# Kernel tuning notes

Hardware: AMD Instinct MI355X
Metric: run time of the kernel (lower is better)

## Reference

```python
import jax, jax.numpy as jnp
import numpy as np

B, S, H, E, K, NH = 2, 2048, 1024, 8, 2, 8
HD = H // NH          # head dim = 128
HQ = H // 4           # seasonal encoder width = 256
CAP = int(B * S * 1.5 * K / E)  # expert capacity = 1536


def setup_inputs() -> dict:
    key = jax.random.key(0)
    ks = iter(jax.random.split(key, 32))

    def lin(shape):
        fan_in = shape[0]
        return jax.random.normal(next(ks), shape, jnp.float32) / np.sqrt(fan_in)

    inp = {
        "hidden_states": jax.random.normal(next(ks), (B, S, H), jnp.float32),
        # position embedding table [sequence_length, H]
        "pos_emb": jax.random.normal(next(ks), (S, H), jnp.float32) * 0.02,
        # temporal_encoder: Linear(H+2,H) -> ReLU -> Linear(H,H)
        "We1": lin((H + 2, H)), "be1": jnp.zeros((H,), jnp.float32),
        "We2": lin((H, H)),     "be2": jnp.zeros((H,), jnp.float32),
        # seasonal_encoder: Linear(1,H//4) -> ReLU -> Linear(H//4,H//4)
        "Ws1": lin((1, HQ)),   "bs1": jnp.zeros((HQ,), jnp.float32),
        "Ws2": lin((HQ, HQ)),  "bs2": jnp.zeros((HQ,), jnp.float32),
        # temporal_attention (MultiheadAttention, 8 heads)
        "Wq": lin((H, H)), "bq": jnp.zeros((H,), jnp.float32),
        "Wk": lin((H, H)), "bk": jnp.zeros((H,), jnp.float32),
        "Wv": lin((H, H)), "bv": jnp.zeros((H,), jnp.float32),
        "Wo": lin((H, H)), "bo": jnp.zeros((H,), jnp.float32),
        # temporal_router: Linear(H,H) -> ReLU -> Linear(H,E)
        "Wr1": lin((H, H)), "br1": jnp.zeros((H,), jnp.float32),
        "Wr2": lin((H, E)), "br2": jnp.zeros((E,), jnp.float32),
    }
    return inp


def _forward(hidden_states, pos_emb, We1, be1, We2, be2, Ws1, bs1, Ws2, bs2,
             Wq, bq, Wk, bk, Wv, bv, Wo, bo, Wr1, br1, Wr2, br2):
    b, s, h = hidden_states.shape
    # time features (time_info is None -> defaults)
    t = jnp.arange(s, dtype=jnp.float32)                   # [S]
    season = jnp.sin(t * 2.0 * jnp.pi / 24.0)              # [S]
    time_feat = jnp.broadcast_to(jnp.stack([t, season], -1), (b, s, 2))

    combined = jnp.concatenate([hidden_states, time_feat], axis=-1)  # [B,S,H+2]
    enc = jax.nn.relu(combined @ We1 + be1) @ We2 + be2              # [B,S,H]

    pos = pos_emb[:s]                                                # [S,H]
    seas = jax.nn.relu(season[:, None] @ Ws1 + bs1) @ Ws2 + bs2      # [S,H//4]
    seas_full = jnp.tile(seas, (1, h // seas.shape[-1]))             # [S,H] (expand to H)

    x = enc + pos[None] + seas_full[None]                            # [B,S,H]

    # self-attention (eval mode, no dropout)
    def heads(y):
        return y.reshape(b, s, NH, HD)
    q = heads(x @ Wq + bq)
    k = heads(x @ Wk + bk)
    v = heads(x @ Wv + bv)
    scores = jnp.einsum('bqhd,bkhd->bhqk', q, k) / np.sqrt(HD)
    attn = jax.nn.softmax(scores, axis=-1)
    ctx = jnp.einsum('bhqk,bkhd->bqhd', attn, v).reshape(b, s, h)
    x = ctx @ Wo + bo

    logits = jax.nn.relu(x @ Wr1 + br1) @ Wr2 + br2                  # [B,S,E]
    probs = jax.nn.softmax(logits, axis=-1)

    topv, topi = jax.lax.top_k(probs, K)                             # [B,S,K]
    topv = topv / topv.sum(-1, keepdims=True)

    onehot = jax.nn.one_hot(topi, E, dtype=probs.dtype)              # [B,S,K,E]
    disp0 = onehot.sum(-2)                                           # [B,S,E] (0/1)
    comb0 = (topv[..., None] * onehot).sum(-2)                       # [B,S,E]

    # only capacity slot 0 is ever written (per original code)
    dispatch = jnp.zeros((b, s, E, CAP), probs.dtype).at[..., 0].set(disp0)
    combine = jnp.zeros((b, s, E, CAP), probs.dtype).at[..., 0].set(comb0)

    p_mean = probs.mean(axis=(0, 1))                                 # [E]
    aux_loss = jnp.sum(p_mean * jnp.log(p_mean * E + 1e-9))
    return dispatch, combine, probs, aux_loss


def reference(hidden_states, pos_emb, We1, be1, We2, be2, Ws1, bs1, Ws2, bs2,
              Wq, bq, Wk, bk, Wv, bv, Wo, bo, Wr1, br1, Wr2, br2):
    return _forward(hidden_states, pos_emb, We1, be1, We2, be2, Ws1, bs1, Ws2, bs2,
                    Wq, bq, Wk, bk, Wv, bv, Wo, bo, Wr1, br1, Wr2, br2)
```

## Files before the change

### kernel.cpp

```cpp
#include <hip/hip_runtime.h>
#include <hip/hip_fp16.h>
#include <math.h>

#define N_TOK 4096
#define S_LEN 2048
#define H_DIM 1024
#define E_EXP 8
#define CAPV  1536
#define NHEAD 8
#define HDHD  128

#define SCRATCH_F4 2129920u
#define TOTAL_F4   25165824u

typedef __attribute__((ext_vector_type(8))) _Float16 v8h;
typedef __attribute__((ext_vector_type(4))) float v4f;

__device__ __forceinline__ void splitf16(float v, unsigned short& h, unsigned short& l) {
    __half hh = __float2half(v);
    h = __half_as_ushort(hh);
    l = __half_as_ushort(__float2half(v - __half2float(hh)));
}

__device__ __forceinline__ void gld_lds16(const void* g, void* l) {
    __builtin_amdgcn_global_load_lds(
        (const __attribute__((address_space(1))) unsigned int*)g,
        (__attribute__((address_space(3))) unsigned int*)l,
        16, 0, 0);
}

__global__ __launch_bounds__(256) void prep_k(
    const float* __restrict__ hid, unsigned short* __restrict__ hi,
    unsigned short* __restrict__ lo,
    const float* __restrict__ Ws1, const float* __restrict__ bs1,
    const float* __restrict__ Ws2, const float* __restrict__ bs2,
    float* __restrict__ seasons, float* __restrict__ seas24,
    const float* __restrict__ Wr2, float* __restrict__ wr2t) {
    __shared__ float hbuf[256];
    int blk = blockIdx.x;
    int tid = threadIdx.x;
    if (blk < 4096) {
        int i = blk * 256 + tid;
        float4 v = ((const float4*)hid)[i];
        ushort4 h, l;
        splitf16(v.x, h.x, l.x);
        splitf16(v.y, h.y, l.y);
        splitf16(v.z, h.z, l.z);
        splitf16(v.w, h.w, l.w);
        ((ushort4*)hi)[i] = h;
        ((ushort4*)lo)[i] = l;
    } else if (blk < 4104) {
        int s = (blk - 4096) * 256 + tid;
        if (s < S_LEN) {
            double a = (double)s * 2.0 * M_PI / 24.0;
            seasons[s] = (float)sin(a);
        }
    } else if (blk < 4128) {
        int m = blk - 4104;
        double a = (double)m * 2.0 * M_PI / 24.0;
        float sv = (float)sin(a);
        int j = tid;
        hbuf[j] = fmaxf(sv * Ws1[j] + bs1[j], 0.f);
        __syncthreads();
        float acc = bs2[j];
        for (int i = 0; i < 256; ++i) acc = fmaf(hbuf[i], Ws2[i * 256 + j], acc);
        seas24[m * 256 + j] = acc;
    } else {
        int i = (blk - 4128) * 256 + tid;
        int k = i >> 3, e = i & 7;
        wr2t[e * 1024 + k] = Wr2[i];
    }
}

__device__ __forceinline__ void wconv_body(const float* __restrict__ W,
                                           unsigned short* __restrict__ Thi,
                                           unsigned short* __restrict__ Tlo) {
    __shared__ unsigned short Hs[64][65];
    __shared__ unsigned short Ls[64][65];
    int k0 = blockIdx.y * 64, n0 = blockIdx.x * 64;
    int tid = threadIdx.x;
#pragma unroll
    for (int i = 0; i < 4; ++i) {
        int idx = tid + i * 256;
        int kk = idx >> 4, n4 = idx & 15;
        float4 v = *(const float4*)(W + (size_t)(k0 + kk) * 1024 + n0 + n4 * 4);
        unsigned short h, l;
        splitf16(v.x, h, l); Hs[n4 * 4 + 0][kk] = h; Ls[n4 * 4 + 0][kk] = l;
        splitf16(v.y, h, l); Hs[n4 * 4 + 1][kk] = h; Ls[n4 * 4 + 1][kk] = l;
        splitf16(v.z, h, l); Hs[n4 * 4 + 2][kk] = h; Ls[n4 * 4 + 2][kk] = l;
        splitf16(v.w, h, l); Hs[n4 * 4 + 3][kk] = h; Ls[n4 * 4 + 3][kk] = l;
    }
    __syncthreads();
#pragma unroll
    for (int i = 0; i < 4; ++i) {
        int idx = tid + i * 256;
        int n = idx >> 4, k4 = idx & 15;
        ushort4 h = make_ushort4(Hs[n][k4 * 4], Hs[n][k4 * 4 + 1], Hs[n][k4 * 4 + 2], Hs[n][k4 * 4 + 3]);
        ushort4 l = make_ushort4(Ls[n][k4 * 4], Ls[n][k4 * 4 + 1], Ls[n][k4 * 4 + 2], Ls[n][k4 * 4 + 3]);
        *(ushort4*)(Thi + (size_t)(n0 + n) * 1024 + k0 + k4 * 4) = h;
        *(ushort4*)(Tlo + (size_t)(n0 + n) * 1024 + k0 + k4 * 4) = l;
    }
}

struct WBatch {
    const float* src[7];
    unsigned short* dh[7];
    unsigned short* dl[7];
};

__global__ __launch_bounds__(256) void wconv_batch_k(WBatch wb) {
    int i = blockIdx.z;
    wconv_body(wb.src[i], wb.dh[i], wb.dl[i]);
}

__device__ __forceinline__ void fill_body(float* __restrict__ p, size_t f40, size_t f41, int nblk) {
    v4f z = {0.f, 0.f, 0.f, 0.f};
    v4f* o = (v4f*)p;
    size_t n = f41 - f40;
    for (size_t i = (size_t)blockIdx.x * 256 + threadIdx.x; i < n; i += (size_t)nblk * 256)
        __builtin_nontemporal_store(z, o + f40 + i);
}

template <int MODE, int EMITF, int EMITS, int FILLN>
__global__ __launch_bounds__(256, 2) void gemm_split(
    const unsigned short* __restrict__ Ahi, const unsigned short* __restrict__ Alo,
    const unsigned short* __restrict__ WThi, const unsigned short* __restrict__ WTlo,
    const float* __restrict__ bias, float* __restrict__ Cf,
    unsigned short* __restrict__ Chi, unsigned short* __restrict__ Clo,
    const float* __restrict__ rowT, const float* __restrict__ rowS,
    const float* __restrict__ seasons, const float* __restrict__ pos,
    const float* __restrict__ seas24, float escale, float* __restrict__ fillp) {
    if (FILLN > 0) {
        if (blockIdx.x < (unsigned)FILLN) {
            fill_body(fillp, 0, SCRATCH_F4, FILLN);
            return;
        }
    }
    __shared__ unsigned short Ash[2][128 * 32];
    __shared__ unsigned short Asl[2][128 * 32];
    __shared__ unsigned short Bsh[2][128 * 32];
    __shared__ unsigned short Bsl[2][128 * 32];
    int tid = threadIdx.x;
    int lane = tid & 63, w = tid >> 6;
    int l15 = lane & 15, l16 = lane >> 4;
    int wm = (w >> 1) * 64, wn = (w & 1) * 64;

    int bid = blockIdx.x - FILLN;
    int mp = (bid & 7) + ((bid >> 6) << 3);
    int np = (bid >> 3) & 7;
    int m0 = mp * 128, n0 = np * 128;

    int ac0 = tid, ac1 = tid + 256;
    int ar0 = ac0 >> 2, ar1 = ac1 >> 2;
    size_t a_src0 = (size_t)(m0 + ar0) * 1024 + (((ac0 & 3) ^ (ar0 & 3)) * 8);
    size_t a_src1 = (size_t)(m0 + ar1) * 1024 + (((ac1 & 3) ^ (ar1 & 3)) * 8);
    size_t b_src0 = (size_t)(n0 + ar0) * 1024 + (((ac0 & 3) ^ (ar0 & 3)) * 8);
    size_t b_src1 = (size_t)(n0 + ar1) * 1024 + (((ac1 & 3) ^ (ar1 & 3)) * 8);

    int a_off[4], b_off[4];
#pragma unroll
    for (int mi = 0; mi < 4; ++mi) {
        int row = wm + mi * 16 + l15;
        a_off[mi] = row * 32 + ((l16 ^ (row & 3)) * 8);
    }
#pragma unroll
    for (int ni = 0; ni < 4; ++ni) {
        int n = wn + ni * 16 + l15;
        b_off[ni] = n * 32 + ((l16 ^ (n & 3)) * 8);
    }

    auto STAGE = [&](int buf, int k0) {
        gld_lds16(Ahi + a_src0 + k0, &Ash[buf][ac0 * 8]);
        gld_lds16(Ahi + a_src1 + k0, &Ash[buf][ac1 * 8]);
        gld_lds16(Alo + a_src0 + k0, &Asl[buf][ac0 * 8]);
        gld_lds16(Alo + a_src1 + k0, &Asl[buf][ac1 * 8]);
        gld_lds16(WThi + b_src0 + k0, &Bsh[buf][ac0 * 8]);
        gld_lds16(WThi + b_src1 + k0, &Bsh[buf][ac1 * 8]);
        gld_lds16(WTlo + b_src0 + k0, &Bsl[buf][ac0 * 8]);
        gld_lds16(WTlo + b_src1 + k0, &Bsl[buf][ac1 * 8]);
    };

    v4f acc[4][4] = {};
    STAGE(0, 0);
    __syncthreads();

    for (int kk = 0; kk < 32; ++kk) {
        int cur = kk & 1;
        if (kk < 31) STAGE(cur ^ 1, (kk + 1) * 32);
        v8h ah[4], al[4], bh[4], bl[4];
#pragma unroll
        for (int mi = 0; mi < 4; ++mi) {
            ah[mi] = *(const v8h*)&Ash[cur][a_off[mi]];
            al[mi] = *(const v8h*)&Asl[cur][a_off[mi]];
        }
#pragma unroll
        for (int ni = 0; ni < 4; ++ni) {
            bh[ni] = *(const v8h*)&Bsh[cur][b_off[ni]];
            bl[ni] = *(const v8h*)&Bsl[cur][b_off[ni]];
        }
#pragma unroll
        for (int mi = 0; mi < 4; ++mi)
#pragma unroll
            for (int ni = 0; ni < 4; ++ni) {
                acc[mi][ni] = __builtin_amdgcn_mfma_f32_16x16x32_f16(ah[mi], bh[ni], acc[mi][ni], 0, 0, 0);
                acc[mi][ni] = __builtin_amdgcn_mfma_f32_16x16x32_f16(al[mi], bh[ni], acc[mi][ni], 0, 0, 0);
                acc[mi][ni] = __builtin_amdgcn_mfma_f32_16x16x32_f16(ah[mi], bl[ni], acc[mi][ni], 0, 0, 0);
            }
        __syncthreads();
    }

#pragma unroll
    for (int mi = 0; mi < 4; ++mi) {
#pragma unroll
        for (int r = 0; r < 4; ++r) {
            int row = m0 + wm + mi * 16 + l16 * 4 + r;
            int s = row & (S_LEN - 1);
            float tval = 0.f, seval = 0.f;
            if (MODE == 1) { tval = (float)s; seval = seasons[s]; }
#pragma unroll
            for (int ni = 0; ni < 4; ++ni) {
                int col = n0 + wn + ni * 16 + l15;
                float v = acc[mi][ni][r] + bias[col];
                if (MODE == 1) v += tval * rowT[col] + seval * rowS[col];
                if (MODE == 2) v += pos[(size_t)s * 1024 + col] + seas24[(s % 24) * 256 + (col & 255)];
                if (MODE == 1 || MODE == 3) v = fmaxf(v, 0.f);
                size_t o = (size_t)row * 1024 + col;
                if (EMITF) Cf[o] = v;
                if (EMITS) {
                    unsigned short hu, lu;
                    splitf16(v * escale, hu, lu);
                    Chi[o] = hu; Clo[o] = lu;
                }
            }
        }
    }
}

#define NFILLQ 256
__global__ __launch_bounds__(256, 2) void gemm_qkv(
    const unsigned short* __restrict__ Ahi, const unsigned short* __restrict__ Alo,
    const unsigned short* __restrict__ WT3hi, const unsigned short* __restrict__ WT3lo,
    const float* __restrict__ bq, const float* __restrict__ bk,
    const float* __restrict__ bv,
    unsigned short* __restrict__ Qhi, unsigned short* __restrict__ Qlo,
    unsigned short* __restrict__ Khi, unsigned short* __restrict__ Klo,
    unsigned short* __restrict__ VThi, unsigned short* __restrict__ VTlo,
    float qscale, float* __restrict__ fillp) {
    if (blockIdx.x < NFILLQ) {
        fill_body(fillp, SCRATCH_F4, TOTAL_F4, NFILLQ);
        return;
    }
    __shared__ unsigned short Ash[2][128 * 32];
    __shared__ unsigned short Asl[2][128 * 32];
    __shared__ unsigned short Bsh[2][128 * 32];
    __shared__ unsigned short Bsl[2][128 * 32];
    int tid = threadIdx.x;
    int lane = tid & 63, w = tid >> 6;
    int l15 = lane & 15, l16 = lane >> 4;
    int wm = (w >> 1) * 64, wn = (w & 1) * 64;

    int bid = blockIdx.x - NFILLQ;
    int t = bid >> 3;
    int np = t % 24;
    int mp = (bid & 7) + (t / 24) * 8;
    int m0 = mp * 128;
    int wn0 = np * 128;

    int ac0 = tid, ac1 = tid + 256;
    int ar0 = ac0 >> 2, ar1 = ac1 >> 2;
    size_t a_src0 = (size_t)(m0 + ar0) * 1024 + (((ac0 & 3) ^ (ar0 & 3)) * 8);
    size_t a_src1 = (size_t)(m0 + ar1) * 1024 + (((ac1 & 3) ^ (ar1 & 3)) * 8);
    size_t b_src0 = (size_t)(wn0 + ar0) * 1024 + (((ac0 & 3) ^ (ar0 & 3)) * 8);
    size_t b_src1 = (size_t)(wn0 + ar1) * 1024 + (((ac1 & 3) ^ (ar1 & 3)) * 8);

    int a_off[4], b_off[4];
#pragma unroll
    for (int mi = 0; mi < 4; ++mi) {
        int row = wm + mi * 16 + l15;
        a_off[mi] = row * 32 + ((l16 ^ (row & 3)) * 8);
    }
#pragma unroll
    for (int ni = 0; ni < 4; ++ni) {
        int n = wn + ni * 16 + l15;
        b_off[ni] = n * 32 + ((l16 ^ (n & 3)) * 8);
    }

    auto STAGE = [&](int buf, int k0) {
        gld_lds16(Ahi + a_src0 + k0, &Ash[buf][ac0 * 8]);
        gld_lds16(Ahi + a_src1 + k0, &Ash[buf][ac1 * 8]);
        gld_lds16(Alo + a_src0 + k0, &Asl[buf][ac0 * 8]);
        gld_lds16(Alo + a_src1 + k0, &Asl[buf][ac1 * 8]);
        gld_lds16(WT3hi + b_src0 + k0, &Bsh[buf][ac0 * 8]);
        gld_lds16(WT3hi + b_src1 + k0, &Bsh[buf][ac1 * 8]);
        gld_lds16(WT3lo + b_src0 + k0, &Bsl[buf][ac0 * 8]);
        gld_lds16(WT3lo + b_src1 + k0, &Bsl[buf][ac1 * 8]);
    };

    v4f acc[4][4] = {};
    STAGE(0, 0);
    __syncthreads();

    for (int kk = 0; kk < 32; ++kk) {
        int cur = kk & 1;
        if (kk < 31) STAGE(cur ^ 1, (kk + 1) * 32);
        v8h ah[4], al[4], bh[4], bl[4];
#pragma unroll
        for (int mi = 0; mi < 4; ++mi) {
            ah[mi] = *(const v8h*)&Ash[cur][a_off[mi]];
            al[mi] = *(const v8h*)&Asl[cur][a_off[mi]];
        }
#pragma unroll
        for (int ni = 0; ni < 4; ++ni) {
            bh[ni] = *(const v8h*)&Bsh[cur][b_off[ni]];
            bl[ni] = *(const v8h*)&Bsl[cur][b_off[ni]];
        }
#pragma unroll
        for (int mi = 0; mi < 4; ++mi)
#pragma unroll
            for (int ni = 0; ni < 4; ++ni) {
                acc[mi][ni] = __builtin_amdgcn_mfma_f32_16x16x32_f16(ah[mi], bh[ni], acc[mi][ni], 0, 0, 0);
                acc[mi][ni] = __builtin_amdgcn_mfma_f32_16x16x32_f16(al[mi], bh[ni], acc[mi][ni], 0, 0, 0);
                acc[mi][ni] = __builtin_amdgcn_mfma_f32_16x16x32_f16(ah[mi], bl[ni], acc[mi][ni], 0, 0, 0);
            }
        __syncthreads();
    }

    if (np >= 16) {
        int n0 = (np - 16) * 128;
#pragma unroll
        for (int mi = 0; mi < 4; ++mi) {
            int row0 = m0 + wm + mi * 16 + l16 * 4;
            int bb = row0 >> 11, ss = row0 & 2047;
#pragma unroll
            for (int ni = 0; ni < 4; ++ni) {
                int col = n0 + wn + ni * 16 + l15;
                int hh = col >> 7, dd = col & 127;
                size_t base = ((size_t)((bb * 8 + hh) * 128 + dd)) * 2048 + ss;
                ushort4 vh, vl;
                float v0 = acc[mi][ni][0] + bv[col];
                float v1 = acc[mi][ni][1] + bv[col];
                float v2 = acc[mi][ni][2] + bv[col];
                float v3 = acc[mi][ni][3] + bv[col];
                splitf16(v0, vh.x, vl.x);
                splitf16(v1, vh.y, vl.y);
                splitf16(v2, vh.z, vl.z);
                splitf16(v3, vh.w, vl.w);
                *(ushort4*)(VThi + base) = vh;
                *(ushort4*)(VTlo + base) = vl;
            }
        }
    } else {
        const float* bias = np < 8 ? bq : bk;
        unsigned short* Dhi = np < 8 ? Qhi : Khi;
        unsigned short* Dlo = np < 8 ? Qlo : Klo;
        float esc = np < 8 ? qscale : 1.f;
        int n0 = (np & 7) * 128;
#pragma unroll
        for (int mi = 0; mi < 4; ++mi) {
#pragma unroll
            for (int r = 0; r < 4; ++r) {
                int row = m0 + wm + mi * 16 + l16 * 4 + r;
#pragma unroll
                for (int ni = 0; ni < 4; ++ni) {
                    int col = n0 + wn + ni * 16 + l15;
                    float v = (acc[mi][ni][r] + bias[col]) * esc;
                    size_t o = (size_t)row * 1024 + col;
                    unsigned short hu, lu;
                    splitf16(v, hu, lu);
                    Dhi[o] = hu; Dlo[o] = lu;
                }
            }
        }
    }
}

__global__ __launch_bounds__(256, 4) void attn_mfma_k(
    const unsigned short* __restrict__ qhi, const unsigned short* __restrict__ qlo,
    const unsigned short* __restrict__ khi, const unsigned short* __restrict__ klo,
    const unsigned short* __restrict__ vthi, const unsigned short* __restrict__ vtlo,
    float* __restrict__ OP, float* __restrict__ ML) {
    __shared__ unsigned short Ks_hi[32 * 128];
    __shared__ unsigned short Ks_lo[32 * 128];
    __shared__ unsigned short Vs_hi[128 * 32];
    __shared__ unsigned short Vs_lo[128 * 32];
    __shared__ unsigned int   Ps[64 * 32];

    int p = blockIdx.x;
    int x = (p >> 3) & 31;
    int g = (p & 7) + ((p >> 8) << 3);
    int bh = g >> 1, z = g & 1;
    int b = bh >> 3, h = bh & 7;
    int q0 = x * 64;
    int tid = threadIdx.x;
    int lane = tid & 63, w = tid >> 6;
    int l15 = lane & 15, l16 = lane >> 4;
    int wm = w * 16;

    v8h qa_h[4], qa_l[4];
    {
        size_t qrow = (size_t)(b * S_LEN + q0 + wm + l15) * H_DIM + h * HDHD;
#pragma unroll
        for (int ks = 0; ks < 4; ++ks) {
            qa_h[ks] = *(const v8h*)(qhi + qrow + ks * 32 + l16 * 8);
            qa_l[ks] = *(const v8h*)(qlo + qrow + ks * 32 + l16 * 8);
        }
    }

    int ktok1 = tid >> 4, kslot1 = tid & 15;
    int ktok2 = ktok1 + 16;
    size_t ksrc1 = (size_t)(b * S_LEN + ktok1) * H_DIM + h * HDHD + ((kslot1 ^ (ktok1 & 7)) * 8);
    size_t ksrc2 = (size_t)(b * S_LEN + ktok2) * H_DIM + h * HDHD + ((kslot1 ^ (ktok2 & 7)) * 8);
    int vd1 = tid >> 2, vslot1 = tid & 3;
    int vd2 = vd1 + 64;
    size_t vsrc1 = (size_t)(bh * HDHD + vd1) * S_LEN + ((vslot1 ^ ((vd1 >> 1) & 3)) * 8);
    size_t vsrc2 = (size_t)(bh * HDHD + vd2) * S_LEN + ((vslot1 ^ ((vd2 >> 1) & 3)) * 8);

    v4f accO[8] = {};
    float mreg[4] = {-1e30f, -1e30f, -1e30f, -1e30f};
    float lreg[4] = {};

    int kt0 = z * 1024;
    for (int it = 0; it < 32; ++it) {
        int kt = kt0 + it * 32;
        __syncthreads();
        size_t koff = (size_t)kt * H_DIM;
        gld_lds16(khi + ksrc1 + koff, &Ks_hi[tid * 8]);
        gld_lds16(khi + ksrc2 + koff, &Ks_hi[(tid + 256) * 8]);
        gld_lds16(klo + ksrc1 + koff, &Ks_lo[tid * 8]);
        gld_lds16(klo + ksrc2 + koff, &Ks_lo[(tid + 256) * 8]);
        gld_lds16(vthi + vsrc1 + kt, &Vs_hi[tid * 8]);
        gld_lds16(vthi + vsrc2 + kt, &Vs_hi[(tid + 256) * 8]);
        gld_lds16(vtlo + vsrc1 + kt, &Vs_lo[tid * 8]);
        gld_lds16(vtlo + vsrc2 + kt, &Vs_lo[(tid + 256) * 8]);
        __syncthreads();

        v4f s0 = {}, s1 = {};
#pragma unroll
        for (int ks = 0; ks < 4; ++ks) {
#pragma unroll
            for (int nt = 0; nt < 2; ++nt) {
                int tok = nt * 16 + l15;
                int slot = (ks * 4 + l16) ^ (tok & 7);
                v8h bhf = *(const v8h*)&Ks_hi[tok * 128 + slot * 8];
                v8h blf = *(const v8h*)&Ks_lo[tok * 128 + slot * 8];
                v4f& ss = nt ? s1 : s0;
                ss = __builtin_amdgcn_mfma_f32_16x16x32_f16(qa_h[ks], bhf, ss, 0, 0, 0);
                ss = __builtin_amdgcn_mfma_f32_16x16x32_f16(qa_l[ks], bhf, ss, 0, 0, 0);
                ss = __builtin_amdgcn_mfma_f32_16x16x32_f16(qa_h[ks], blf, ss, 0, 0, 0);
            }
        }

        float p0[4], p1[4], alpha[4];
#pragma unroll
        for (int r = 0; r < 4; ++r) {
            float tmax = fmaxf(s0[r], s1[r]);
            tmax = fmaxf(tmax, __shfl_xor(tmax, 1));
            tmax = fmaxf(tmax, __shfl_xor(tmax, 2));
            tmax = fmaxf(tmax, __shfl_xor(tmax, 4));
            tmax = fmaxf(tmax, __shfl_xor(tmax, 8));
            float mnew = fmaxf(mreg[r], tmax);
            alpha[r] = __expf(mreg[r] - mnew);
            p0[r] = __expf(s0[r] - mnew);
            p1[r] = __expf(s1[r] - mnew);
            float lt = p0[r] + p1[r];
            lt += __shfl_xor(lt, 1);
            lt += __shfl_xor(lt, 2);
            lt += __shfl_xor(lt, 4);
            lt += __shfl_xor(lt, 8);
            lreg[r] = lreg[r] * alpha[r] + lt;
            mreg[r] = mnew;
        }
#pragma unroll
        for (int nt = 0; nt < 8; ++nt)
#pragma unroll
            for (int r = 0; r < 4; ++r) accO[nt][r] *= alpha[r];

#pragma unroll
        for (int r = 0; r < 4; ++r) {
            int qq = wm + l16 * 4 + r;
            unsigned short ph, pl;
            splitf16(p0[r], ph, pl);
            int k0i = l15;
            Ps[qq * 32 + ((((k0i >> 2) ^ (qq & 7)) << 2) | (k0i & 3))] =
                (unsigned)ph | ((unsigned)pl << 16);
            splitf16(p1[r], ph, pl);
            int k1i = 16 + l15;
            Ps[qq * 32 + ((((k1i >> 2) ^ (qq & 7)) << 2) | (k1i & 3))] =
                (unsigned)ph | ((unsigned)pl << 16);
        }

        int qq = wm + l15;
        int sA = (l16 * 2) ^ (qq & 7);
        int sB = (l16 * 2 + 1) ^ (qq & 7);
        uint4 ua = *(const uint4*)&Ps[qq * 32 + sA * 4];
        uint4 ub = *(const uint4*)&Ps[qq * 32 + sB * 4];
        uint4 ahw, alw;
        ahw.x = (ua.x & 0xffffu) | (ua.y << 16);
        ahw.y = (ua.z & 0xffffu) | (ua.w << 16);
        ahw.z = (ub.x & 0xffffu) | (ub.y << 16);
        ahw.w = (ub.z & 0xffffu) | (ub.w << 16);
        alw.x = (ua.x >> 16) | (ua.y & 0xffff0000u);
        alw.y = (ua.z >> 16) | (ua.w & 0xffff0000u);
        alw.z = (ub.x >> 16) | (ub.y & 0xffff0000u);
        alw.w = (ub.z >> 16) | (ub.w & 0xffff0000u);
        v8h pA_h = __builtin_bit_cast(v8h, ahw);
        v8h pA_l = __builtin_bit_cast(v8h, alw);
#pragma unroll
        for (int nt = 0; nt < 8; ++nt) {
            int d = nt * 16 + l15;
            int slot = l16 ^ ((d >> 1) & 3);
            v8h vhf = *(const v8h*)&Vs_hi[d * 32 + slot * 8];
            v8h vlf = *(const v8h*)&Vs_lo[d * 32 + slot * 8];
            accO[nt] = __builtin_amdgcn_mfma_f32_16x16x32_f16(pA_h, vhf, accO[nt], 0, 0, 0);
            accO[nt] = __builtin_amdgcn_mfma_f32_16x16x32_f16(pA_l, vhf, accO[nt], 0, 0, 0);
            accO[nt] = __builtin_amdgcn_mfma_f32_16x16x32_f16(pA_h, vlf, accO[nt], 0, 0, 0);
        }
    }

#pragma unroll
    for (int r = 0; r < 4; ++r) {
        if (l15 == 0) {
            int q = q0 + wm + l16 * 4 + r;
            size_t mlo = ((size_t)(z * 16 + bh) * 2048 + q) * 2;
            ML[mlo] = mreg[r];
            ML[mlo + 1] = lreg[r];
        }
    }
#pragma unroll
    for (int nt = 0; nt < 8; ++nt) {
#pragma unroll
        for (int r = 0; r < 4; ++r) {
            int q = q0 + wm + l16 * 4 + r;
            size_t o = ((size_t)(z * 16 + bh) * 2048 + q) * 128 + nt * 16 + l15;
            OP[o] = accO[nt][r];
        }
    }
}

__global__ __launch_bounds__(256) void attn_combine_k(
    const float* __restrict__ OP, const float* __restrict__ ML,
    unsigned short* __restrict__ ctx_hi, unsigned short* __restrict__ ctx_lo) {
    int tid = threadIdx.x;
    int R = blockIdx.x * 16 + (tid >> 4);
    int bh = R >> 11, q = R & 2047;
    int b = bh >> 3, h = bh & 7;
    int d0 = (tid & 15) * 8;
    size_t ml0 = ((size_t)bh * 2048 + q) * 2;
    size_t ml1 = ((size_t)(16 + bh) * 2048 + q) * 2;
    float m0 = ML[ml0], l0 = ML[ml0 + 1];
    float m1 = ML[ml1], l1 = ML[ml1 + 1];
    float m = fmaxf(m0, m1);
    float w0 = __expf(m0 - m), w1 = __expf(m1 - m);
    float inv = 1.f / (w0 * l0 + w1 * l1);
    const float* O0 = OP + ((size_t)bh * 2048 + q) * 128 + d0;
    const float* O1 = OP + ((size_t)(16 + bh) * 2048 + q) * 128 + d0;
    size_t dst = ((size_t)(b * 2048 + q)) * 1024 + h * 128 + d0;
    float4 a0 = *(const float4*)O0;
    float4 a1 = *(const float4*)(O0 + 4);
    float4 c0 = *(const float4*)O1;
    float4 c1 = *(const float4*)(O1 + 4);
    ushort4 h0, h1, lo0, lo1;
    splitf16((w0 * a0.x + w1 * c0.x) * inv, h0.x, lo0.x);
    splitf16((w0 * a0.y + w1 * c0.y) * inv, h0.y, lo0.y);
    splitf16((w0 * a0.z + w1 * c0.z) * inv, h0.z, lo0.z);
    splitf16((w0 * a0.w + w1 * c0.w) * inv, h0.w, lo0.w);
    splitf16((w0 * a1.x + w1 * c1.x) * inv, h1.x, lo1.x);
    splitf16((w0 * a1.y + w1 * c1.y) * inv, h1.y, lo1.y);
    splitf16((w0 * a1.z + w1 * c1.z) * inv, h1.z, lo1.z);
    splitf16((w0 * a1.w + w1 * c1.w) * inv, h1.w, lo1.w);
    *(ushort4*)(ctx_hi + dst) = h0;
    *(ushort4*)(ctx_hi + dst + 4) = h1;
    *(ushort4*)(ctx_lo + dst) = lo0;
    *(ushort4*)(ctx_lo + dst + 4) = lo1;
}

__global__ __launch_bounds__(256) void logits_k(const float* __restrict__ h1,
                                                const float* __restrict__ Wr2T,
                                                const float* __restrict__ br2,
                                                float* __restrict__ logits) {
    __shared__ float part[256];
    int tid = threadIdx.x;
    int tok8 = tid >> 5;
    int e = (tid >> 2) & 7;
    int ch = tid & 3;
    int tok = blockIdx.x * 8 + tok8;
    const float4* h4 = (const float4*)(h1 + (size_t)tok * 1024 + ch * 256);
    const float4* w4 = (const float4*)(Wr2T + (size_t)e * 1024 + ch * 256);
    float acc = 0.f;
#pragma unroll
    for (int i = 0; i < 64; ++i) {
        float4 a = h4[i];
        float4 bb = w4[i];
        acc = fmaf(a.x, bb.x, fmaf(a.y, bb.y, fmaf(a.z, bb.z, fmaf(a.w, bb.w, acc))));
    }
    part[tid] = acc;
    __syncthreads();
    if (ch == 0) {
        float s = part[tid] + part[tid + 1] + part[tid + 2] + part[tid + 3] + br2[e];
        logits[(size_t)tok * 8 + e] = s;
    }
}

__global__ __launch_bounds__(256) void topk_scatter_k(const float* __restrict__ logits,
                                                      float* __restrict__ out) {
    int tok = blockIdx.x * 256 + threadIdx.x;
    if (tok >= N_TOK) return;
    float l[8], p[8];
    float mx = -1e30f;
#pragma unroll
    for (int e = 0; e < 8; ++e) { l[e] = logits[(size_t)tok * 8 + e]; mx = fmaxf(mx, l[e]); }
    float sum = 0.f;
#pragma unroll
    for (int e = 0; e < 8; ++e) { p[e] = __expf(l[e] - mx); sum += p[e]; }
    float inv = 1.f / sum;
#pragma unroll
    for (int e = 0; e < 8; ++e) p[e] *= inv;
    const size_t NEC = (size_t)N_TOK * E_EXP * CAPV;
    float* probs_out = out + 2 * NEC;
#pragma unroll
    for (int e = 0; e < 8; ++e) probs_out[(size_t)tok * 8 + e] = p[e];
    int i1 = 0;
#pragma unroll
    for (int e = 1; e < 8; ++e) if (p[e] > p[i1]) i1 = e;
    int i2 = -1;
#pragma unroll
    for (int e = 0; e < 8; ++e) {
        if (e == i1) continue;
        if (i2 < 0 || p[e] > p[i2]) i2 = e;
    }
    float v1 = p[i1], v2 = p[i2], tv = v1 + v2;
    size_t base = (size_t)tok * E_EXP * CAPV;
    out[base + (size_t)i1 * CAPV] = 1.f;
    out[base + (size_t)i2 * CAPV] = 1.f;
    out[NEC + base + (size_t)i1 * CAPV] = v1 / tv;
    out[NEC + base + (size_t)i2 * CAPV] = v2 / tv;
}

__global__ void aux_k(const float* __restrict__ probs, float* __restrict__ out_aux) {
    __shared__ float part[256];
    int tid = threadIdx.x;
    int e = tid & 7, chunk = tid >> 3;
    float s = 0.f;
    for (int t = chunk * 128; t < (chunk + 1) * 128; ++t)
        s += probs[(size_t)t * 8 + e];
    part[tid] = s;
    __syncthreads();
    if (tid < 8) {
        float tot = 0.f;
        for (int c = 0; c < 32; ++c) tot += part[c * 8 + e];
        part[tid] = tot / (float)N_TOK;
    }
    __syncthreads();
    if (tid == 0) {
        float aux = 0.f;
        for (int e2 = 0; e2 < 8; ++e2) {
            float pm = part[e2];
            aux += pm * logf(pm * 8.f + 1e-9f);
        }
        *out_aux = aux;
    }
}

extern "C" void kernel_launch(void* const* d_in, const int* in_sizes, int n_in,
                              void* d_out, int out_size, void* d_ws, size_t ws_size,
                              hipStream_t stream) {
    const float* hid = (const float*)d_in[0];
    const float* pos = (const float*)d_in[1];
    const float* We1 = (const float*)d_in[2];
    const float* be1 = (const float*)d_in[3];
    const float* We2 = (const float*)d_in[4];
    const float* be2 = (const float*)d_in[5];
    const float* Ws1 = (const float*)d_in[6];
    const float* bs1 = (const float*)d_in[7];
    const float* Ws2 = (const float*)d_in[8];
    const float* bs2 = (const float*)d_in[9];
    const float* Wq  = (const float*)d_in[10]; const float* bq = (const float*)d_in[11];
    const float* Wk  = (const float*)d_in[12]; const float* bk = (const float*)d_in[13];
    const float* Wv  = (const float*)d_in[14]; const float* bv = (const float*)d_in[15];
    const float* Wo  = (const float*)d_in[16]; const float* bo = (const float*)d_in[17];
    const float* Wr1 = (const float*)d_in[18]; const float* br1 = (const float*)d_in[19];
    const float* Wr2 = (const float*)d_in[20]; const float* br2 = (const float*)d_in[21];

    float* out = (float*)d_out;
    char* base = (char*)d_ws;
    const size_t AC  = (size_t)N_TOK * H_DIM;
    const size_t SPC = AC * 2;
    const size_t FB  = AC * 4;
    const size_t MB  = (size_t)1 << 20;

    unsigned short* B1hi = (unsigned short*)(base);
    unsigned short* B1lo = (unsigned short*)(base + SPC);
    unsigned short* B2hi = (unsigned short*)(base + FB);
    unsigned short* B2lo = (unsigned short*)(base + FB + SPC);
    unsigned short* Qhi  = (unsigned short*)(base + 2 * FB);
    unsigned short* Qlo  = (unsigned short*)(base + 2 * FB + SPC);
    unsigned short* Khi  = (unsigned short*)(base + 3 * FB);
    unsigned short* Klo  = (unsigned short*)(base + 3 * FB + SPC);
    unsigned short* VThi = (unsigned short*)(base + 4 * FB);
    unsigned short* VTlo = (unsigned short*)(base + 4 * FB + SPC);
    float* h1f = (float*)(base + 3 * FB);

    char* wp = base + 5 * FB;
    unsigned short* We1hi = (unsigned short*)(wp);
    unsigned short* We1lo = (unsigned short*)(wp + 2 * MB);
    unsigned short* We2hi = (unsigned short*)(wp + 4 * MB);
    unsigned short* We2lo = (unsigned short*)(wp + 6 * MB);
    unsigned short* QKVhi = (unsigned short*)(wp + 8 * MB);
    unsigned short* QKVlo = (unsigned short*)(wp + 14 * MB);
    unsigned short* Wohi  = (unsigned short*)(wp + 20 * MB);
    unsigned short* Wolo  = (unsigned short*)(wp + 22 * MB);
    unsigned short* Wr1hi = (unsigned short*)(wp + 24 * MB);
    unsigned short* Wr1lo = (unsigned short*)(wp + 26 * MB);
    char* smalls = wp + 28 * MB;
    float* wr2t    = (float*)smalls;
    float* seas24  = wr2t + 8192;
    float* seasons = seas24 + 6144;
    float* logits  = seasons + 2048;

    const size_t NEC = (size_t)N_TOK * E_EXP * CAPV;
    const float QSCALE = 0.08838834764831845f;

    float* OP = out;
    float* ML = out + (size_t)2 * 16 * 2048 * 128;

    dim3 blk(256);

    prep_k<<<4160, 256, 0, stream>>>(hid, B1hi, B1lo, Ws1, bs1, Ws2, bs2,
                                     seasons, seas24, Wr2, wr2t);

    WBatch wb;
    wb.src[0] = We1; wb.dh[0] = We1hi; wb.dl[0] = We1lo;
    wb.src[1] = We2; wb.dh[1] = We2hi; wb.dl[1] = We2lo;
    wb.src[2] = Wq;  wb.dh[2] = QKVhi;                        wb.dl[2] = QKVlo;
    wb.src[3] = Wk;  wb.dh[3] = QKVhi + (size_t)1024 * 1024;  wb.dl[3] = QKVlo + (size_t)1024 * 1024;
    wb.src[4] = Wv;  wb.dh[4] = QKVhi + (size_t)2048 * 1024;  wb.dl[4] = QKVlo + (size_t)2048 * 1024;
    wb.src[5] = Wo;  wb.dh[5] = Wohi;  wb.dl[5] = Wolo;
    wb.src[6] = Wr1; wb.dh[6] = Wr1hi; wb.dl[6] = Wr1lo;
    wconv_batch_k<<<dim3(16, 16, 7), blk, 0, stream>>>(wb);

    gemm_split<1, 0, 1, 0><<<256, blk, 0, stream>>>(B1hi, B1lo, We1hi, We1lo, be1,
        nullptr, B2hi, B2lo,
        We1 + (size_t)1024 * 1024, We1 + (size_t)1025 * 1024, seasons, nullptr, nullptr, 1.f, nullptr);
    gemm_split<2, 0, 1, 0><<<256, blk, 0, stream>>>(B2hi, B2lo, We2hi, We2lo, be2,
        nullptr, B1hi, B1lo, nullptr, nullptr, nullptr, pos, seas24, 1.f, nullptr);

    gemm_qkv<<<768 + NFILLQ, blk, 0, stream>>>(B1hi, B1lo, QKVhi, QKVlo, bq, bk, bv,
                                               Qhi, Qlo, Khi, Klo, VThi, VTlo, QSCALE, out);

    attn_mfma_k<<<1024, 256, 0, stream>>>(Qhi, Qlo, Khi, Klo, VThi, VTlo, OP, ML);
    attn_combine_k<<<2048, 256, 0, stream>>>(OP, ML, B2hi, B2lo);

    gemm_split<0, 0, 1, 64><<<256 + 64, blk, 0, stream>>>(B2hi, B2lo, Wohi, Wolo, bo,
        nullptr, B1hi, B1lo, nullptr, nullptr, nullptr, nullptr, nullptr, 1.f, out);
    gemm_split<3, 1, 0, 0><<<256, blk, 0, stream>>>(B1hi, B1lo, Wr1hi, Wr1lo, br1,
        h1f, nullptr, nullptr, nullptr, nullptr, nullptr, nullptr, nullptr, 1.f, nullptr);

    logits_k<<<512, 256, 0, stream>>>(h1f, wr2t, br2, logits);
    topk_scatter_k<<<16, 256, 0, stream>>>(logits, out);
    aux_k<<<1, 256, 0, stream>>>(out + 2 * NEC, out + 2 * NEC + (size_t)N_TOK * E_EXP);
}
```

Measured before the change: 566.5 us.

## Use 512-thread GEMM blocks with smaller per-wave tiles; fuse logits with top-k

Measured after the change: 523.6 us. 7.6% less time.

```diff
diff --git a/kernel.cpp b/kernel.cpp
--- a/kernel.cpp
+++ b/kernel.cpp
@@ -117,12 +117,13 @@
     v4f z = {0.f, 0.f, 0.f, 0.f};
     v4f* o = (v4f*)p;
     size_t n = f41 - f40;
-    for (size_t i = (size_t)blockIdx.x * 256 + threadIdx.x; i < n; i += (size_t)nblk * 256)
+    size_t T = blockDim.x;
+    for (size_t i = (size_t)blockIdx.x * T + threadIdx.x; i < n; i += (size_t)nblk * T)
         __builtin_nontemporal_store(z, o + f40 + i);
 }
 
 template <int MODE, int EMITF, int EMITS, int FILLN>
-__global__ __launch_bounds__(256, 2) void gemm_split(
+__global__ __launch_bounds__(512, 4) void gemm_split(
     const unsigned short* __restrict__ Ahi, const unsigned short* __restrict__ Alo,
     const unsigned short* __restrict__ WThi, const unsigned short* __restrict__ WTlo,
     const float* __restrict__ bias, float* __restrict__ Cf,
@@ -143,23 +144,21 @@
     int tid = threadIdx.x;
     int lane = tid & 63, w = tid >> 6;
     int l15 = lane & 15, l16 = lane >> 4;
-    int wm = (w >> 1) * 64, wn = (w & 1) * 64;
+    int wm = (w >> 1) * 32, wn = (w & 1) * 64;
 
     int bid = blockIdx.x - FILLN;
     int mp = (bid & 7) + ((bid >> 6) << 3);
     int np = (bid >> 3) & 7;
     int m0 = mp * 128, n0 = np * 128;
 
-    int ac0 = tid, ac1 = tid + 256;
-    int ar0 = ac0 >> 2, ar1 = ac1 >> 2;
+    int ac0 = tid;
+    int ar0 = ac0 >> 2;
     size_t a_src0 = (size_t)(m0 + ar0) * 1024 + (((ac0 & 3) ^ (ar0 & 3)) * 8);
-    size_t a_src1 = (size_t)(m0 + ar1) * 1024 + (((ac1 & 3) ^ (ar1 & 3)) * 8);
     size_t b_src0 = (size_t)(n0 + ar0) * 1024 + (((ac0 & 3) ^ (ar0 & 3)) * 8);
-    size_t b_src1 = (size_t)(n0 + ar1) * 1024 + (((ac1 & 3) ^ (ar1 & 3)) * 8);
-
-    int a_off[4], b_off[4];
-#pragma unroll
-    for (int mi = 0; mi < 4; ++mi) {
+
+    int a_off[2], b_off[4];
+#pragma unroll
+    for (int mi = 0; mi < 2; ++mi) {
         int row = wm + mi * 16 + l15;
         a_off[mi] = row * 32 + ((l16 ^ (row & 3)) * 8);
     }
@@ -171,25 +170,21 @@
 
     auto STAGE = [&](int buf, int k0) {
         gld_lds16(Ahi + a_src0 + k0, &Ash[buf][ac0 * 8]);
-        gld_lds16(Ahi + a_src1 + k0, &Ash[buf][ac1 * 8]);
         gld_lds16(Alo + a_src0 + k0, &Asl[buf][ac0 * 8]);
-        gld_lds16(Alo + a_src1 + k0, &Asl[buf][ac1 * 8]);
         gld_lds16(WThi + b_src0 + k0, &Bsh[buf][ac0 * 8]);
-        gld_lds16(WThi + b_src1 + k0, &Bsh[buf][ac1 * 8]);
         gld_lds16(WTlo + b_src0 + k0, &Bsl[buf][ac0 * 8]);
-        gld_lds16(WTlo + b_src1 + k0, &Bsl[buf][ac1 * 8]);
     };
 
-    v4f acc[4][4] = {};
+    v4f acc[2][4] = {};
     STAGE(0, 0);
     __syncthreads();
 
     for (int kk = 0; kk < 32; ++kk) {
         int cur = kk & 1;
         if (kk < 31) STAGE(cur ^ 1, (kk + 1) * 32);
-        v8h ah[4], al[4], bh[4], bl[4];
-#pragma unroll
-        for (int mi = 0; mi < 4; ++mi) {
+        v8h ah[2], al[2], bh[4], bl[4];
+#pragma unroll
+        for (int mi = 0; mi < 2; ++mi) {
             ah[mi] = *(const v8h*)&Ash[cur][a_off[mi]];
             al[mi] = *(const v8h*)&Asl[cur][a_off[mi]];
         }
@@ -199,7 +194,7 @@
             bl[ni] = *(const v8h*)&Bsl[cur][b_off[ni]];
         }
 #pragma unroll
-        for (int mi = 0; mi < 4; ++mi)
+        for (int mi = 0; mi < 2; ++mi)
 #pragma unroll
             for (int ni = 0; ni < 4; ++ni) {
                 acc[mi][ni] = __builtin_amdgcn_mfma_f32_16x16x32_f16(ah[mi], bh[ni], acc[mi][ni], 0, 0, 0);
@@ -210,7 +205,7 @@
     }
 
 #pragma unroll
-    for (int mi = 0; mi < 4; ++mi) {
+    for (int mi = 0; mi < 2; ++mi) {
 #pragma unroll
         for (int r = 0; r < 4; ++r) {
             int row = m0 + wm + mi * 16 + l16 * 4 + r;
@@ -236,8 +231,8 @@
     }
 }
 
-#define NFILLQ 256
-__global__ __launch_bounds__(256, 2) void gemm_qkv(
+#define NFILLQ 128
+__global__ __launch_bounds__(512, 4) void gemm_qkv(
     const unsigned short* __restrict__ Ahi, const unsigned short* __restrict__ Alo,
     const unsigned short* __restrict__ WT3hi, const unsigned short* __restrict__ WT3lo,
     const float* __restrict__ bq, const float* __restrict__ bk,
@@ -257,7 +252,7 @@
     int tid = threadIdx.x;
     int lane = tid & 63, w = tid >> 6;
     int l15 = lane & 15, l16 = lane >> 4;
-    int wm = (w >> 1) * 64, wn = (w & 1) * 64;
+    int wm = (w >> 1) * 32, wn = (w & 1) * 64;
 
     int bid = blockIdx.x - NFILLQ;
     int t = bid >> 3;
@@ -266,16 +261,14 @@
     int m0 = mp * 128;
     int wn0 = np * 128;
 
-    int ac0 = tid, ac1 = tid + 256;
-    int ar0 = ac0 >> 2, ar1 = ac1 >> 2;
+    int ac0 = tid;
+    int ar0 = ac0 >> 2;
     size_t a_src0 = (size_t)(m0 + ar0) * 1024 + (((ac0 & 3) ^ (ar0 & 3)) * 8);
-    size_t a_src1 = (size_t)(m0 + ar1) * 1024 + (((ac1 & 3) ^ (ar1 & 3)) * 8);
     size_t b_src0 = (size_t)(wn0 + ar0) * 1024 + (((ac0 & 3) ^ (ar0 & 3)) * 8);
-    size_t b_src1 = (size_t)(wn0 + ar1) * 1024 + (((ac1 & 3) ^ (ar1 & 3)) * 8);
-
-    int a_off[4], b_off[4];
-#pragma unroll
-    for (int mi = 0; mi < 4; ++mi) {
+
+    int a_off[2], b_off[4];
+#pragma unroll
+    for (int mi = 0; mi < 2; ++mi) {
         int row = wm + mi * 16 + l15;
         a_off[mi] = row * 32 + ((l16 ^ (row & 3)) * 8);
     }
@@ -287,25 +280,21 @@
 
     auto STAGE = [&](int buf, int k0) {
         gld_lds16(Ahi + a_src0 + k0, &Ash[buf][ac0 * 8]);
-        gld_lds16(Ahi + a_src1 + k0, &Ash[buf][ac1 * 8]);
         gld_lds16(Alo + a_src0 + k0, &Asl[buf][ac0 * 8]);
-        gld_lds16(Alo + a_src1 + k0, &Asl[buf][ac1 * 8]);
         gld_lds16(WT3hi + b_src0 + k0, &Bsh[buf][ac0 * 8]);
-        gld_lds16(WT3hi + b_src1 + k0, &Bsh[buf][ac1 * 8]);
         gld_lds16(WT3lo + b_src0 + k0, &Bsl[buf][ac0 * 8]);
-        gld_lds16(WT3lo + b_src1 + k0, &Bsl[buf][ac1 * 8]);
     };
 
-    v4f acc[4][4] = {};
+    v4f acc[2][4] = {};
     STAGE(0, 0);
     __syncthreads();
 
     for (int kk = 0; kk < 32; ++kk) {
         int cur = kk & 1;
         if (kk < 31) STAGE(cur ^ 1, (kk + 1) * 32);
-        v8h ah[4], al[4], bh[4], bl[4];
-#pragma unroll
-        for (int mi = 0; mi < 4; ++mi) {
+        v8h ah[2], al[2], bh[4], bl[4];
+#pragma unroll
+        for (int mi = 0; mi < 2; ++mi) {
             ah[mi] = *(const v8h*)&Ash[cur][a_off[mi]];
             al[mi] = *(const v8h*)&Asl[cur][a_off[mi]];
         }
@@ -315,7 +304,7 @@
             bl[ni] = *(const v8h*)&Bsl[cur][b_off[ni]];
         }
 #pragma unroll
-        for (int mi = 0; mi < 4; ++mi)
+        for (int mi = 0; mi < 2; ++mi)
 #pragma unroll
             for (int ni = 0; ni < 4; ++ni) {
                 acc[mi][ni] = __builtin_amdgcn_mfma_f32_16x16x32_f16(ah[mi], bh[ni], acc[mi][ni], 0, 0, 0);
@@ -328,7 +317,7 @@
     if (np >= 16) {
         int n0 = (np - 16) * 128;
 #pragma unroll
-        for (int mi = 0; mi < 4; ++mi) {
+        for (int mi = 0; mi < 2; ++mi) {
             int row0 = m0 + wm + mi * 16 + l16 * 4;
             int bb = row0 >> 11, ss = row0 & 2047;
 #pragma unroll
@@ -356,7 +345,7 @@
         float esc = np < 8 ? qscale : 1.f;
         int n0 = (np & 7) * 128;
 #pragma unroll
-        for (int mi = 0; mi < 4; ++mi) {
+        for (int mi = 0; mi < 2; ++mi) {
 #pragma unroll
             for (int r = 0; r < 4; ++r) {
                 int row = m0 + wm + mi * 16 + l16 * 4 + r;
@@ -574,11 +563,12 @@
     *(ushort4*)(ctx_lo + dst + 4) = lo1;
 }
 
-__global__ __launch_bounds__(256) void logits_k(const float* __restrict__ h1,
-                                                const float* __restrict__ Wr2T,
-                                                const float* __restrict__ br2,
-                                                float* __restrict__ logits) {
+__global__ __launch_bounds__(256) void logits_topk_k(const float* __restrict__ h1,
+                                                     const float* __restrict__ Wr2T,
+                                                     const float* __restrict__ br2,
+                                                     float* __restrict__ out) {
     __shared__ float part[256];
+    __shared__ float lg[8][8];
     int tid = threadIdx.x;
     int tok8 = tid >> 5;
     int e = (tid >> 2) & 7;
@@ -595,45 +585,41 @@
     }
     part[tid] = acc;
     __syncthreads();
-    if (ch == 0) {
-        float s = part[tid] + part[tid + 1] + part[tid + 2] + part[tid + 3] + br2[e];
-        logits[(size_t)tok * 8 + e] = s;
-    }
-}
-
-__global__ __launch_bounds__(256) void topk_scatter_k(const float* __restrict__ logits,
-                                                      float* __restrict__ out) {
-    int tok = blockIdx.x * 256 + threadIdx.x;
-    if (tok >= N_TOK) return;
-    float l[8], p[8];
-    float mx = -1e30f;
-#pragma unroll
-    for (int e = 0; e < 8; ++e) { l[e] = logits[(size_t)tok * 8 + e]; mx = fmaxf(mx, l[e]); }
-    float sum = 0.f;
-#pragma unroll
-    for (int e = 0; e < 8; ++e) { p[e] = __expf(l[e] - mx); sum += p[e]; }
-    float inv = 1.f / sum;
-#pragma unroll
-    for (int e = 0; e < 8; ++e) p[e] *= inv;
-    const size_t NEC = (size_t)N_TOK * E_EXP * CAPV;
-    float* probs_out = out + 2 * NEC;
-#pragma unroll
-    for (int e = 0; e < 8; ++e) probs_out[(size_t)tok * 8 + e] = p[e];
-    int i1 = 0;
-#pragma unroll
-    for (int e = 1; e < 8; ++e) if (p[e] > p[i1]) i1 = e;
-    int i2 = -1;
-#pragma unroll
-    for (int e = 0; e < 8; ++e) {
-        if (e == i1) continue;
-        if (i2 < 0 || p[e] > p[i2]) i2 = e;
-    }
-    float v1 = p[i1], v2 = p[i2], tv = v1 + v2;
-    size_t base = (size_t)tok * E_EXP * CAPV;
-    out[base + (size_t)i1 * CAPV] = 1.f;
-    out[base + (size_t)i2 * CAPV] = 1.f;
-    out[NEC + base + (size_t)i1 * CAPV] = v1 / tv;
-    out[NEC + base + (size_t)i2 * CAPV] = v2 / tv;
+    if (ch == 0)
+        lg[tok8][e] = part[tid] + part[tid + 1] + part[tid + 2] + part[tid + 3] + br2[e];
+    __syncthreads();
+    if (tid < 8) {
+        int myTok = blockIdx.x * 8 + tid;
+        float l[8], p[8];
+        float mx = -1e30f;
+#pragma unroll
+        for (int k = 0; k < 8; ++k) { l[k] = lg[tid][k]; mx = fmaxf(mx, l[k]); }
+        float sum = 0.f;
+#pragma unroll
+        for (int k = 0; k < 8; ++k) { p[k] = __expf(l[k] - mx); sum += p[k]; }
+        float inv = 1.f / sum;
+#pragma unroll
+        for (int k = 0; k < 8; ++k) p[k] *= inv;
+        const size_t NEC = (size_t)N_TOK * E_EXP * CAPV;
+        float* probs_out = out + 2 * NEC;
+#pragma unroll
+        for (int k = 0; k < 8; ++k) probs_out[(size_t)myTok * 8 + k] = p[k];
+        int i1 = 0;
+#pragma unroll
+        for (int k = 1; k < 8; ++k) if (p[k] > p[i1]) i1 = k;
+        int i2 = -1;
+#pragma unroll
+        for (int k = 0; k < 8; ++k) {
+            if (k == i1) continue;
+            if (i2 < 0 || p[k] > p[i2]) i2 = k;
+        }
+        float v1 = p[i1], v2 = p[i2], tv = v1 + v2;
+        size_t base = (size_t)myTok * E_EXP * CAPV;
+        out[base + (size_t)i1 * CAPV] = 1.f;
+        out[base + (size_t)i2 * CAPV] = 1.f;
+        out[NEC + base + (size_t)i1 * CAPV] = v1 / tv;
+        out[NEC + base + (size_t)i2 * CAPV] = v2 / tv;
+    }
 }
 
 __global__ void aux_k(const float* __restrict__ probs, float* __restrict__ out_aux) {
@@ -715,7 +701,6 @@
     float* wr2t    = (float*)smalls;
     float* seas24  = wr2t + 8192;
     float* seasons = seas24 + 6144;
-    float* logits  = seasons + 2048;
 
     const size_t NEC = (size_t)N_TOK * E_EXP * CAPV;
     const float QSCALE = 0.08838834764831845f;
@@ -723,9 +708,9 @@
     float* OP = out;
     float* ML = out + (size_t)2 * 16 * 2048 * 128;
 
-    dim3 blk(256);
-
-    prep_k<<<4160, 256, 0, stream>>>(hid, B1hi, B1lo, Ws1, bs1, Ws2, bs2,
+    dim3 blk(256), blk512(512);
+
+    prep_k<<<4160, blk, 0, stream>>>(hid, B1hi, B1lo, Ws1, bs1, Ws2, bs2,
                                      seasons, seas24, Wr2, wr2t);
 
     WBatch wb;
@@ -738,24 +723,23 @@
     wb.src[6] = Wr1; wb.dh[6] = Wr1hi; wb.dl[6] = Wr1lo;
     wconv_batch_k<<<dim3(16, 16, 7), blk, 0, stream>>>(wb);
 
-    gemm_split<1, 0, 1, 0><<<256, blk, 0, stream>>>(B1hi, B1lo, We1hi, We1lo, be1,
+    gemm_split<1, 0, 1, 0><<<256, blk512, 0, stream>>>(B1hi, B1lo, We1hi, We1lo, be1,
         nullptr, B2hi, B2lo,
         We1 + (size_t)1024 * 1024, We1 + (size_t)1025 * 1024, seasons, nullptr, nullptr, 1.f, nullptr);
-    gemm_split<2, 0, 1, 0><<<256, blk, 0, stream>>>(B2hi, B2lo, We2hi, We2lo, be2,
+    gemm_split<2, 0, 1, 0><<<256, blk512, 0, stream>>>(B2hi, B2lo, We2hi, We2lo, be2,
         nullptr, B1hi, B1lo, nullptr, nullptr, nullptr, pos, seas24, 1.f, nullptr);
 
-    gemm_qkv<<<768 + NFILLQ, blk, 0, stream>>>(B1hi, B1lo, QKVhi, QKVlo, bq, bk, bv,
-                                               Qhi, Qlo, Khi, Klo, VThi, VTlo, QSCALE, out);
-
-    attn_mfma_k<<<1024, 256, 0, stream>>>(Qhi, Qlo, Khi, Klo, VThi, VTlo, OP, ML);
-    attn_combine_k<<<2048, 256, 0, stream>>>(OP, ML, B2hi, B2lo);
-
-    gemm_split<0, 0, 1, 64><<<256 + 64, blk, 0, stream>>>(B2hi, B2lo, Wohi, Wolo, bo,
+    gemm_qkv<<<768 + NFILLQ, blk512, 0, stream>>>(B1hi, B1lo, QKVhi, QKVlo, bq, bk, bv,
+                                                  Qhi, Qlo, Khi, Klo, VThi, VTlo, QSCALE, out);
+
+    attn_mfma_k<<<1024, blk, 0, stream>>>(Qhi, Qlo, Khi, Klo, VThi, VTlo, OP, ML);
+    attn_combine_k<<<2048, blk, 0, stream>>>(OP, ML, B2hi, B2lo);
+
+    gemm_split<0, 0, 1, 32><<<256 + 32, blk512, 0, stream>>>(B2hi, B2lo, Wohi, Wolo, bo,
         nullptr, B1hi, B1lo, nullptr, nullptr, nullptr, nullptr, nullptr, 1.f, out);
-    gemm_split<3, 1, 0, 0><<<256, blk, 0, stream>>>(B1hi, B1lo, Wr1hi, Wr1lo, br1,
+    gemm_split<3, 1, 0, 0><<<256, blk512, 0, stream>>>(B1hi, B1lo, Wr1hi, Wr1lo, br1,
         h1f, nullptr, nullptr, nullptr, nullptr, nullptr, nullptr, nullptr, 1.f, nullptr);
 
-    logits_k<<<512, 256, 0, stream>>>(h1f, wr2t, br2, logits);
-    topk_scatter_k<<<16, 256, 0, stream>>>(logits, out);
-    aux_k<<<1, 256, 0, stream>>>(out + 2 * NEC, out + 2 * NEC + (size_t)N_TOK * E_EXP);
-}
+    logits_topk_k<<<512, blk, 0, stream>>>(h1f, wr2t, br2, out);
+    aux_k<<<1, blk, 0, stream>>>(out + 2 * NEC, out + 2 * NEC + (size_t)N_TOK * E_EXP);
+}
```
